# Performance work log

Hardware: AMD Instinct MI355X
Metric: run time of the kernel (lower is better)

## Reference

```python
import jax, jax.numpy as jnp
import numpy as np

N, E = 50000, 800000
IN, HID, HEADS, OUT = 128, 16, 4, 40
NEG_SLOPE = 0.2
BN_EPS = 1e-5


def gat_conv(x, edge_src, edge_dst, W, a_src, a_dst, b, heads, out_ch, concat):
    """PyG GATConv: linear -> per-head attention logits -> segment softmax over
    incoming edges of each target node -> weighted scatter-sum. Self-loops are
    assumed already appended to edge_src/edge_dst."""
    n = x.shape[0]
    h = (x @ W.T).reshape(n, heads, out_ch)              # [N, H, C]
    alpha_s = jnp.sum(h * a_src, axis=-1)                # [N, H]
    alpha_d = jnp.sum(h * a_dst, axis=-1)                # [N, H]
    logits = jax.nn.leaky_relu(alpha_s[edge_src] + alpha_d[edge_dst], NEG_SLOPE)  # [E', H]
    # numerically-stable segment softmax over edges grouped by target node
    seg_max = jax.ops.segment_max(logits, edge_dst, num_segments=n)
    e = jnp.exp(logits - seg_max[edge_dst])
    seg_sum = jax.ops.segment_sum(e, edge_dst, num_segments=n)
    alpha = e / (seg_sum[edge_dst] + 1e-16)              # [E', H]
    msg = h[edge_src] * alpha[:, :, None]                # [E', H, C]
    out = jax.ops.segment_sum(msg, edge_dst, num_segments=n)  # [N, H, C]
    out = out.reshape(n, heads * out_ch) if concat else out.mean(axis=1)
    return out + b


def batch_norm(x, gamma, beta):
    mean = x.mean(axis=0)
    var = x.var(axis=0)  # biased, matching torch BN normalization
    return (x - mean) * jax.lax.rsqrt(var + BN_EPS) * gamma + beta


def setup_inputs() -> dict:
    key = jax.random.key(0)
    ks = jax.random.split(key, 16)
    H = HID * HEADS  # 64
    inp = {
        "x": jax.random.normal(ks[0], (N, IN), jnp.float32),
        "edge_index": jax.random.randint(ks[1], (2, E), 0, N, jnp.int64),
        # layer 0: IN -> HID, HEADS heads, concat
        "W0": jax.random.normal(ks[2], (H, IN), jnp.float32) * 0.05,
        "a_src0": jax.random.normal(ks[3], (1, HEADS, HID), jnp.float32) * 0.05,
        "a_dst0": jax.random.normal(ks[4], (1, HEADS, HID), jnp.float32) * 0.05,
        "b0": jnp.zeros((H,), jnp.float32),
        # layer 1: H -> HID, HEADS heads, concat
        "W1": jax.random.normal(ks[5], (H, H), jnp.float32) * 0.05,
        "a_src1": jax.random.normal(ks[6], (1, HEADS, HID), jnp.float32) * 0.05,
        "a_dst1": jax.random.normal(ks[7], (1, HEADS, HID), jnp.float32) * 0.05,
        "b1": jnp.zeros((H,), jnp.float32),
        # layer 2: H -> OUT, 1 head, concat=False
        "W2": jax.random.normal(ks[8], (OUT, H), jnp.float32) * 0.05,
        "a_src2": jax.random.normal(ks[9], (1, 1, OUT), jnp.float32) * 0.05,
        "a_dst2": jax.random.normal(ks[10], (1, 1, OUT), jnp.float32) * 0.05,
        "b2": jnp.zeros((OUT,), jnp.float32),
        # batchnorms
        "g0": jnp.ones((H,), jnp.float32), "bt0": jnp.zeros((H,), jnp.float32),
        "g1": jnp.ones((H,), jnp.float32), "bt1": jnp.zeros((H,), jnp.float32),
    }
    return inp


def reference(x, edge_index, W0, a_src0, a_dst0, b0, W1, a_src1, a_dst1, b1,
              W2, a_src2, a_dst2, b2, g0, bt0, g1, bt1):
    n = x.shape[0]
    loop = jnp.arange(n, dtype=edge_index.dtype)
    src = jnp.concatenate([edge_index[0], loop])  # PyG add_self_loops=True
    dst = jnp.concatenate([edge_index[1], loop])

    h = gat_conv(x, src, dst, W0, a_src0, a_dst0, b0, HEADS, HID, True)
    h = batch_norm(h, g0, bt0)
    h = gat_conv(h, src, dst, W1, a_src1, a_dst1, b1, HEADS, HID, True)
    h = batch_norm(h, g1, bt1)
    emb = gat_conv(h, src, dst, W2, a_src2, a_dst2, b2, 1, OUT, False)
    return jax.nn.log_softmax(emb, axis=1), emb
```

## Files before the change

### kernel.cpp

```cpp
#include <hip/hip_runtime.h>
#include <hip/hip_bf16.h>
#include <math.h>

#define NN 50000
#define NE 800000
#define CURPAD 16
#define CAP 64

using short8 = __attribute__((ext_vector_type(8))) short;
using f32x4  = __attribute__((ext_vector_type(4))) float;

__device__ inline short bfbits(float f) {
    __hip_bfloat16 b = __float2bfloat16(f);
    return __builtin_bit_cast(short, b);
}
__device__ inline short8 cvt8(float4 lo, float4 hi) {
    short8 r;
    r[0] = bfbits(lo.x); r[1] = bfbits(lo.y); r[2] = bfbits(lo.z); r[3] = bfbits(lo.w);
    r[4] = bfbits(hi.x); r[5] = bfbits(hi.y); r[6] = bfbits(hi.z); r[7] = bfbits(hi.w);
    return r;
}

template<int K, int CT, int COUT, int HEADSN, bool FUSESCAT>
__global__ __launch_bounds__(256) void mfma_gemm(
    const float* __restrict__ x, const float* __restrict__ W,
    const float* __restrict__ a_src, const float* __restrict__ a_dst,
    const float* __restrict__ bnsc, const float* __restrict__ bnsh,
    ushort* __restrict__ h, float* __restrict__ as_out, float* __restrict__ ad_out,
    int n, int scat_blocks,
    const int* __restrict__ esrc, const int* __restrict__ edst,
    int* __restrict__ cnt, unsigned* __restrict__ pk2)
{
    if (FUSESCAT && (int)blockIdx.x < scat_blocks) {
        int base = ((int)blockIdx.x * 256 + (int)threadIdx.x) * 8;
        int d[8], pv[8];
#pragma unroll
        for (int j = 0; j < 8; j++)
            d[j] = (base + j < NE) ? edst[base + j] : -1;
#pragma unroll
        for (int j = 0; j < 8; j++)
            pv[j] = (d[j] >= 0) ? atomicAdd(&cnt[(size_t)d[j] * CURPAD], 1) : 0;
#pragma unroll
        for (int j = 0; j < 8; j++)
            if (d[j] >= 0 && pv[j] < CAP)
                pk2[((size_t)d[j] << 6) + pv[j]] = (unsigned)esrc[base + j];
        return;
    }

    int bid = (int)blockIdx.x - (FUSESCAT ? scat_blocks : 0);
    int tid = threadIdx.x;
    int w = tid >> 6, l = tid & 63;
    int l15 = l & 15, g = l >> 4;
    int m_base = bid * 64 + w * 16;

    f32x4 acc[CT];
#pragma unroll
    for (int ct = 0; ct < CT; ct++) acc[ct] = f32x4{0.f, 0.f, 0.f, 0.f};

    int arow = m_base + l15; if (arow >= n) arow = n - 1;
    const float* xrow = x + (size_t)arow * K;

#pragma unroll
    for (int ks = 0; ks < K / 32; ks++) {
        int k0 = ks * 32 + g * 8;
        float4 lo = *(const float4*)(xrow + k0);
        float4 hi = *(const float4*)(xrow + k0 + 4);
        if (bnsc) {
            float4 s0 = *(const float4*)(bnsc + k0), s1 = *(const float4*)(bnsc + k0 + 4);
            float4 t0 = *(const float4*)(bnsh + k0), t1 = *(const float4*)(bnsh + k0 + 4);
            lo.x = lo.x * s0.x + t0.x; lo.y = lo.y * s0.y + t0.y;
            lo.z = lo.z * s0.z + t0.z; lo.w = lo.w * s0.w + t0.w;
            hi.x = hi.x * s1.x + t1.x; hi.y = hi.y * s1.y + t1.y;
            hi.z = hi.z * s1.z + t1.z; hi.w = hi.w * s1.w + t1.w;
        }
        short8 a = cvt8(lo, hi);
#pragma unroll
        for (int ct = 0; ct < CT; ct++) {
            int wrow = ct * 16 + l15;
            if (wrow >= COUT) wrow = COUT - 1;
            const float* Wr = W + (size_t)wrow * K;
            float4 blo = *(const float4*)(Wr + k0);
            float4 bhi = *(const float4*)(Wr + k0 + 4);
            short8 b = cvt8(blo, bhi);
            acc[ct] = __builtin_amdgcn_mfma_f32_16x16x32_bf16(a, b, acc[ct], 0, 0, 0);
        }
    }

#pragma unroll
    for (int ct = 0; ct < CT; ct++) {
#pragma unroll
        for (int r = 0; r < 4; r++) {
            int row = m_base + g * 4 + r;
            int col = ct * 16 + l15;
            if (row < n && col < COUT)
                h[(size_t)row * COUT + col] = (ushort)bfbits(acc[ct][r]);
        }
    }

    if (HEADSN == 4) {
        float asv[CT], adv[CT];
#pragma unroll
        for (int ct = 0; ct < CT; ct++) {
            asv[ct] = a_src[ct * 16 + l15];
            adv[ct] = a_dst[ct * 16 + l15];
        }
#pragma unroll
        for (int r = 0; r < 4; r++) {
            float rs[CT], rd[CT];
#pragma unroll
            for (int ct = 0; ct < CT; ct++) {
                rs[ct] = acc[ct][r] * asv[ct];
                rd[ct] = acc[ct][r] * adv[ct];
            }
#pragma unroll
            for (int off = 1; off < 16; off <<= 1) {
#pragma unroll
                for (int ct = 0; ct < CT; ct++) {
                    rs[ct] += __shfl_xor(rs[ct], off);
                    rd[ct] += __shfl_xor(rd[ct], off);
                }
            }
            int row = m_base + g * 4 + r;
            if (row < n) {
#pragma unroll
                for (int ct = 0; ct < CT; ct++) {
                    if (l15 == ct) {
                        as_out[row * 4 + ct] = rs[ct];
                        ad_out[row * 4 + ct] = rd[ct];
                    }
                }
            }
        }
    } else {
        float asv[CT], adv[CT];
#pragma unroll
        for (int ct = 0; ct < CT; ct++) {
            int col = ct * 16 + l15;
            asv[ct] = (col < COUT) ? a_src[col] : 0.f;
            adv[ct] = (col < COUT) ? a_dst[col] : 0.f;
        }
#pragma unroll
        for (int r = 0; r < 4; r++) {
            float rs = 0.f, rd = 0.f;
#pragma unroll
            for (int ct = 0; ct < CT; ct++) {
                rs += acc[ct][r] * asv[ct];
                rd += acc[ct][r] * adv[ct];
            }
#pragma unroll
            for (int off = 1; off < 16; off <<= 1) {
                rs += __shfl_xor(rs, off);
                rd += __shfl_xor(rd, off);
            }
            int row = m_base + g * 4 + r;
            if (row < n && l15 == 0) {
                as_out[row] = rs;
                ad_out[row] = rd;
            }
        }
    }
}

template<int CH, int HEADSN, bool LSM>
__global__ __launch_bounds__(256) void gat_kernel(
    const ushort* __restrict__ h, const float* __restrict__ as,
    const float* __restrict__ ad, const int* __restrict__ cnt,
    const unsigned* __restrict__ pk2, const float* __restrict__ bias,
    float* __restrict__ out, int n)
{
    int wid = (blockIdx.x * blockDim.x + threadIdx.x) >> 6;
    int lane = threadIdx.x & 63;
    if (wid >= n) return;
    int sub = lane & 7, eslot = lane >> 3;
    int c0 = sub * 8;
    bool act = (c0 < CH);
    int hd = (HEADSN == 1) ? 0 : (sub >> 1);
    float adi = ad[wid * HEADSN + hd];

    double ac0 = 0, ac1 = 0, ac2 = 0, ac3 = 0, ac4 = 0, ac5 = 0, ac6 = 0, ac7 = 0;
    double ss = 0;

    int deg = cnt[(size_t)wid * CURPAD];
    if (deg > CAP) deg = CAP;
    int slotbase = wid << 6;
    int nit = (deg + 7) >> 3;
    int pos = eslot;
    bool ok = pos < deg;
    int s = 0; float av = 0.f;
    if (ok) { s = (int)pk2[slotbase + pos]; av = as[s * HEADSN + hd]; }
    for (int it = 0; it < nit; ++it) {
        int posn = pos + 8;
        bool ok2 = (it + 1 < nit) && (posn < deg);
        int s2 = 0; float av2 = 0.f;
        if (ok2) { s2 = (int)pk2[slotbase + posn]; av2 = as[s2 * HEADSN + hd]; }
        float p = 0.f;
        if (ok) {
            float lg = av + adi;
            lg = (lg > 0.f) ? lg : 0.2f * lg;
            p = __expf(fminf(lg, 60.f));
        }
        float h0 = 0.f, h1 = 0.f, h2 = 0.f, h3 = 0.f, h4 = 0.f, h5 = 0.f, h6 = 0.f, h7 = 0.f;
        if (act) {
            uint4 u = *(const uint4*)&h[(size_t)s * CH + c0];
            h0 = __uint_as_float((u.x & 0xffffu) << 16);
            h1 = __uint_as_float(u.x & 0xffff0000u);
            h2 = __uint_as_float((u.y & 0xffffu) << 16);
            h3 = __uint_as_float(u.y & 0xffff0000u);
            h4 = __uint_as_float((u.z & 0xffffu) << 16);
            h5 = __uint_as_float(u.z & 0xffff0000u);
            h6 = __uint_as_float((u.w & 0xffffu) << 16);
            h7 = __uint_as_float(u.w & 0xffff0000u);
        }
        ss += (double)p;
        ac0 += (double)p * (double)h0;  ac1 += (double)p * (double)h1;
        ac2 += (double)p * (double)h2;  ac3 += (double)p * (double)h3;
        ac4 += (double)p * (double)h4;  ac5 += (double)p * (double)h5;
        ac6 += (double)p * (double)h6;  ac7 += (double)p * (double)h7;
        s = s2; av = av2; ok = ok2; pos = posn;
    }

#pragma unroll
    for (int o = 8; o <= 32; o <<= 1) {
        ss  += __shfl_xor(ss, o);
        ac0 += __shfl_xor(ac0, o);  ac1 += __shfl_xor(ac1, o);
        ac2 += __shfl_xor(ac2, o);  ac3 += __shfl_xor(ac3, o);
        ac4 += __shfl_xor(ac4, o);  ac5 += __shfl_xor(ac5, o);
        ac6 += __shfl_xor(ac6, o);  ac7 += __shfl_xor(ac7, o);
    }

    {
        float lg = as[wid * HEADSN + hd] + adi;
        lg = (lg > 0.f) ? lg : 0.2f * lg;
        float ps = __expf(fminf(lg, 60.f));
        ss += (double)ps;
        if (act) {
            uint4 u = *(const uint4*)&h[(size_t)wid * CH + c0];
            ac0 += (double)ps * (double)__uint_as_float((u.x & 0xffffu) << 16);
            ac1 += (double)ps * (double)__uint_as_float(u.x & 0xffff0000u);
            ac2 += (double)ps * (double)__uint_as_float((u.y & 0xffffu) << 16);
            ac3 += (double)ps * (double)__uint_as_float(u.y & 0xffff0000u);
            ac4 += (double)ps * (double)__uint_as_float((u.z & 0xffffu) << 16);
            ac5 += (double)ps * (double)__uint_as_float(u.z & 0xffff0000u);
            ac6 += (double)ps * (double)__uint_as_float((u.w & 0xffffu) << 16);
            ac7 += (double)ps * (double)__uint_as_float(u.w & 0xffff0000u);
        }
    }

    double inv = 1.0 / (ss + 1e-16);
    float4 bv0 = make_float4(0.f, 0.f, 0.f, 0.f), bv1 = bv0;
    if (act) {
        bv0 = *(const float4*)&bias[c0];
        bv1 = *(const float4*)&bias[c0 + 4];
    }
    float v0 = (float)(ac0 * inv) + bv0.x;
    float v1 = (float)(ac1 * inv) + bv0.y;
    float v2 = (float)(ac2 * inv) + bv0.z;
    float v3 = (float)(ac3 * inv) + bv0.w;
    float v4 = (float)(ac4 * inv) + bv1.x;
    float v5 = (float)(ac5 * inv) + bv1.y;
    float v6 = (float)(ac6 * inv) + bv1.z;
    float v7 = (float)(ac7 * inv) + bv1.w;

    if (LSM) {
        float mx = act ? fmaxf(fmaxf(fmaxf(v0, v1), fmaxf(v2, v3)),
                               fmaxf(fmaxf(v4, v5), fmaxf(v6, v7))) : -INFINITY;
        for (int o = 4; o >= 1; o >>= 1) mx = fmaxf(mx, __shfl_xor(mx, o));
        float sse = 0.f;
        if (act)
            sse = __expf(v0 - mx) + __expf(v1 - mx) + __expf(v2 - mx) + __expf(v3 - mx)
                + __expf(v4 - mx) + __expf(v5 - mx) + __expf(v6 - mx) + __expf(v7 - mx);
        for (int o = 4; o >= 1; o >>= 1) sse += __shfl_xor(sse, o);
        float ls = logf(sse);
        if (eslot == 0 && act) {
            *(float4*)&out[(size_t)wid * CH + c0] =
                make_float4(v0 - mx - ls, v1 - mx - ls, v2 - mx - ls, v3 - mx - ls);
            *(float4*)&out[(size_t)wid * CH + c0 + 4] =
                make_float4(v4 - mx - ls, v5 - mx - ls, v6 - mx - ls, v7 - mx - ls);
            *(float4*)&out[(size_t)n * CH + (size_t)wid * CH + c0] =
                make_float4(v0, v1, v2, v3);
            *(float4*)&out[(size_t)n * CH + (size_t)wid * CH + c0 + 4] =
                make_float4(v4, v5, v6, v7);
        }
    } else {
        if (eslot == 0 && act) {
            *(float4*)&out[(size_t)wid * CH + c0] = make_float4(v0, v1, v2, v3);
            *(float4*)&out[(size_t)wid * CH + c0 + 4] = make_float4(v4, v5, v6, v7);
        }
    }
}

__global__ __launch_bounds__(256) void bn_stats(const float* __restrict__ B,
                                                float* __restrict__ psum,
                                                float* __restrict__ psq, int n) {
    __shared__ float ls[256], ls2[256];
    int tid = threadIdx.x;
    int c = tid & 63, r = tid >> 6;
    float s = 0.f, s2 = 0.f;
    for (int i = blockIdx.x * 4 + r; i < n; i += gridDim.x * 4) {
        float v = B[i * 64 + c];
        s += v; s2 += v * v;
    }
    ls[tid] = s; ls2[tid] = s2;
    __syncthreads();
    if (tid < 64) {
        s  = ls[tid] + ls[tid + 64] + ls[tid + 128] + ls[tid + 192];
        s2 = ls2[tid] + ls2[tid + 64] + ls2[tid + 128] + ls2[tid + 192];
        psum[blockIdx.x * 64 + tid] = s;
        psq[blockIdx.x * 64 + tid]  = s2;
    }
}

__global__ void bn_final(const float* __restrict__ psum, const float* __restrict__ psq,
                         const float* __restrict__ g, const float* __restrict__ bt,
                         float* __restrict__ sc, float* __restrict__ sh, int n) {
    int c = threadIdx.x;
    float s = 0.f, s2 = 0.f;
    for (int b = 0; b < 256; b++) {
        s  += psum[b * 64 + c];
        s2 += psq[b * 64 + c];
    }
    float mean = s / n;
    float var = s2 / n - mean * mean;
    float inv = rsqrtf(var + 1e-5f);
    float scale = g[c] * inv;
    sc[c] = scale;
    sh[c] = bt[c] - mean * scale;
}

extern "C" void kernel_launch(void* const* d_in, const int* in_sizes, int n_in,
                              void* d_out, int out_size, void* d_ws, size_t ws_size,
                              hipStream_t stream) {
    const float* x   = (const float*)d_in[0];
    const int*   ei  = (const int*)d_in[1];
    const float* W0  = (const float*)d_in[2];
    const float* as0 = (const float*)d_in[3];
    const float* ad0 = (const float*)d_in[4];
    const float* b0  = (const float*)d_in[5];
    const float* W1  = (const float*)d_in[6];
    const float* as1 = (const float*)d_in[7];
    const float* ad1 = (const float*)d_in[8];
    const float* b1  = (const float*)d_in[9];
    const float* W2  = (const float*)d_in[10];
    const float* as2 = (const float*)d_in[11];
    const float* ad2 = (const float*)d_in[12];
    const float* b2  = (const float*)d_in[13];
    const float* g0  = (const float*)d_in[14];
    const float* bt0 = (const float*)d_in[15];
    const float* g1  = (const float*)d_in[16];
    const float* bt1 = (const float*)d_in[17];

    const int* esrc = ei;
    const int* edst = ei + NE;

    char* ws = (char*)d_ws;
    size_t off = 0;
    auto alloc = [&](size_t bytes) {
        void* p = ws + off;
        off += (bytes + 255) & ~(size_t)255;
        return p;
    };
    int* cnt      = (int*)alloc((size_t)NN * CURPAD * 4);
    unsigned* pk2 = (unsigned*)alloc((size_t)NN * CAP * 4);
    ushort* hbuf  = (ushort*)alloc((size_t)NN * 64 * 2);
    float* obuf   = (float*)alloc((size_t)NN * 64 * 4);
    float* asb    = (float*)alloc((size_t)NN * 4 * 4);
    float* adb    = (float*)alloc((size_t)NN * 4 * 4);
    float* psum   = (float*)alloc(256 * 64 * 4);
    float* psq    = (float*)alloc(256 * 64 * 4);
    float* sc     = (float*)alloc(64 * 4);
    float* sh     = (float*)alloc(64 * 4);

    const int SCB = (NE + 2047) / 2048;
    const int GBM = (NN + 63) / 64;
    const int GB4 = (NN + 3) / 4;

    hipMemsetAsync(cnt, 0, (size_t)NN * CURPAD * 4, stream);
    mfma_gemm<128, 4, 64, 4, true><<<SCB + GBM, 256, 0, stream>>>(
        x, W0, as0, ad0, nullptr, nullptr, hbuf, asb, adb, NN, SCB,
        esrc, edst, cnt, pk2);

    gat_kernel<64, 4, false><<<GB4, 256, 0, stream>>>(hbuf, asb, adb, cnt, pk2,
                                                      b0, obuf, NN);

    bn_stats<<<256, 256, 0, stream>>>(obuf, psum, psq, NN);
    bn_final<<<1, 64, 0, stream>>>(psum, psq, g0, bt0, sc, sh, NN);

    mfma_gemm<64, 4, 64, 4, false><<<GBM, 256, 0, stream>>>(
        obuf, W1, as1, ad1, sc, sh, hbuf, asb, adb, NN, 0,
        nullptr, nullptr, nullptr, nullptr);
    gat_kernel<64, 4, false><<<GB4, 256, 0, stream>>>(hbuf, asb, adb, cnt, pk2,
                                                      b1, obuf, NN);

    bn_stats<<<256, 256, 0, stream>>>(obuf, psum, psq, NN);
    bn_final<<<1, 64, 0, stream>>>(psum, psq, g1, bt1, sc, sh, NN);

    mfma_gemm<64, 3, 40, 1, false><<<GBM, 256, 0, stream>>>(
        obuf, W2, as2, ad2, sc, sh, hbuf, asb, adb, NN, 0,
        nullptr, nullptr, nullptr, nullptr);
    gat_kernel<40, 1, true><<<GB4, 256, 0, stream>>>(hbuf, asb, adb, cnt, pk2,
                                                     b2, (float*)d_out, NN);
}
```

Before: 251.6 us.

## Fuse BN stats into GAT aggregation, widen per-lane channels to sixteen

Batch-norm partial sums are now computed inside the GAT aggregation kernel through shared memory. This removes the separate bn_stats pass over the 50000x64 output, and a new 64-block bn_reduce combines the per-block partials. The aggregation kernel now gives each lane 16 channels (4 lanes per node, 16 edge slots per iteration) instead of 8 channels across 8 slots, which doubles the edge parallelism per wave but also doubles the double-precision accumulator registers. The edge-source load in the scatter is hoisted next to the destination load. The trade-offs are higher register pressure, fewer channels active for the 40-channel layer (the last lane idles), and a grid that assumes N is divisible by 4.

New measurement: 386.6 us. 53.7% more time.

```diff
diff --git a/kernel.cpp b/kernel.cpp
--- a/kernel.cpp
+++ b/kernel.cpp
@@ -33,17 +33,19 @@
 {
     if (FUSESCAT && (int)blockIdx.x < scat_blocks) {
         int base = ((int)blockIdx.x * 256 + (int)threadIdx.x) * 8;
-        int d[8], pv[8];
-#pragma unroll
-        for (int j = 0; j < 8; j++)
+        int d[8], sv[8], pv[8];
+#pragma unroll
+        for (int j = 0; j < 8; j++) {
             d[j] = (base + j < NE) ? edst[base + j] : -1;
+            sv[j] = (base + j < NE) ? esrc[base + j] : 0;
+        }
 #pragma unroll
         for (int j = 0; j < 8; j++)
             pv[j] = (d[j] >= 0) ? atomicAdd(&cnt[(size_t)d[j] * CURPAD], 1) : 0;
 #pragma unroll
         for (int j = 0; j < 8; j++)
             if (d[j] >= 0 && pv[j] < CAP)
-                pk2[((size_t)d[j] << 6) + pv[j]] = (unsigned)esrc[base + j];
+                pk2[((size_t)d[j] << 6) + pv[j]] = (unsigned)sv[j];
         return;
     }
 
@@ -161,35 +163,44 @@
     }
 }
 
-template<int CH, int HEADSN, bool LSM>
+__device__ inline float bfh(unsigned u, bool hi) {
+    return __uint_as_float(hi ? (u & 0xffff0000u) : ((u & 0xffffu) << 16));
+}
+
+template<int CH, int HEADSN, bool LSM, bool BNP>
 __global__ __launch_bounds__(256) void gat_kernel(
     const ushort* __restrict__ h, const float* __restrict__ as,
     const float* __restrict__ ad, const int* __restrict__ cnt,
     const unsigned* __restrict__ pk2, const float* __restrict__ bias,
-    float* __restrict__ out, int n)
+    float* __restrict__ out, float* __restrict__ psum, float* __restrict__ psq,
+    int n)
 {
-    int wid = (blockIdx.x * blockDim.x + threadIdx.x) >> 6;
-    int lane = threadIdx.x & 63;
-    if (wid >= n) return;
-    int sub = lane & 7, eslot = lane >> 3;
-    int c0 = sub * 8;
-    bool act = (c0 < CH);
-    int hd = (HEADSN == 1) ? 0 : (sub >> 1);
+    __shared__ float lsv[4][64];
+    int tid = threadIdx.x;
+    int w = tid >> 6;
+    int wid = blockIdx.x * 4 + w;
+    int lane = tid & 63;
+    int sub = lane & 3, eslot = lane >> 2;
+    int c0 = sub * 16;
+    bool act0 = (c0 < CH), act1 = (c0 + 8 < CH);
+    int hd = (HEADSN == 1) ? 0 : sub;
     float adi = ad[wid * HEADSN + hd];
 
-    double ac0 = 0, ac1 = 0, ac2 = 0, ac3 = 0, ac4 = 0, ac5 = 0, ac6 = 0, ac7 = 0;
-    double ss = 0;
+    double acc[16];
+#pragma unroll
+    for (int j = 0; j < 16; j++) acc[j] = 0.0;
+    double ss = 0.0;
 
     int deg = cnt[(size_t)wid * CURPAD];
     if (deg > CAP) deg = CAP;
     int slotbase = wid << 6;
-    int nit = (deg + 7) >> 3;
+    int nit = (deg + 15) >> 4;
     int pos = eslot;
     bool ok = pos < deg;
     int s = 0; float av = 0.f;
     if (ok) { s = (int)pk2[slotbase + pos]; av = as[s * HEADSN + hd]; }
     for (int it = 0; it < nit; ++it) {
-        int posn = pos + 8;
+        int posn = pos + 16;
         bool ok2 = (it + 1 < nit) && (posn < deg);
         int s2 = 0; float av2 = 0.f;
         if (ok2) { s2 = (int)pk2[slotbase + posn]; av2 = as[s2 * HEADSN + hd]; }
@@ -199,33 +210,26 @@
             lg = (lg > 0.f) ? lg : 0.2f * lg;
             p = __expf(fminf(lg, 60.f));
         }
-        float h0 = 0.f, h1 = 0.f, h2 = 0.f, h3 = 0.f, h4 = 0.f, h5 = 0.f, h6 = 0.f, h7 = 0.f;
-        if (act) {
-            uint4 u = *(const uint4*)&h[(size_t)s * CH + c0];
-            h0 = __uint_as_float((u.x & 0xffffu) << 16);
-            h1 = __uint_as_float(u.x & 0xffff0000u);
-            h2 = __uint_as_float((u.y & 0xffffu) << 16);
-            h3 = __uint_as_float(u.y & 0xffff0000u);
-            h4 = __uint_as_float((u.z & 0xffffu) << 16);
-            h5 = __uint_as_float(u.z & 0xffff0000u);
-            h6 = __uint_as_float((u.w & 0xffffu) << 16);
-            h7 = __uint_as_float(u.w & 0xffff0000u);
-        }
+        uint4 ua = make_uint4(0, 0, 0, 0), ub = ua;
+        if (act0) ua = *(const uint4*)&h[(size_t)s * CH + c0];
+        if (act1) ub = *(const uint4*)&h[(size_t)s * CH + c0 + 8];
         ss += (double)p;
-        ac0 += (double)p * (double)h0;  ac1 += (double)p * (double)h1;
-        ac2 += (double)p * (double)h2;  ac3 += (double)p * (double)h3;
-        ac4 += (double)p * (double)h4;  ac5 += (double)p * (double)h5;
-        ac6 += (double)p * (double)h6;  ac7 += (double)p * (double)h7;
+        acc[0] += (double)p * (double)bfh(ua.x, 0); acc[1] += (double)p * (double)bfh(ua.x, 1);
+        acc[2] += (double)p * (double)bfh(ua.y, 0); acc[3] += (double)p * (double)bfh(ua.y, 1);
+        acc[4] += (double)p * (double)bfh(ua.z, 0); acc[5] += (double)p * (double)bfh(ua.z, 1);
+        acc[6] += (double)p * (double)bfh(ua.w, 0); acc[7] += (double)p * (double)bfh(ua.w, 1);
+        acc[8] += (double)p * (double)bfh(ub.x, 0); acc[9] += (double)p * (double)bfh(ub.x, 1);
+        acc[10] += (double)p * (double)bfh(ub.y, 0); acc[11] += (double)p * (double)bfh(ub.y, 1);
+        acc[12] += (double)p * (double)bfh(ub.z, 0); acc[13] += (double)p * (double)bfh(ub.z, 1);
+        acc[14] += (double)p * (double)bfh(ub.w, 0); acc[15] += (double)p * (double)bfh(ub.w, 1);
         s = s2; av = av2; ok = ok2; pos = posn;
     }
 
 #pragma unroll
-    for (int o = 8; o <= 32; o <<= 1) {
-        ss  += __shfl_xor(ss, o);
-        ac0 += __shfl_xor(ac0, o);  ac1 += __shfl_xor(ac1, o);
-        ac2 += __shfl_xor(ac2, o);  ac3 += __shfl_xor(ac3, o);
-        ac4 += __shfl_xor(ac4, o);  ac5 += __shfl_xor(ac5, o);
-        ac6 += __shfl_xor(ac6, o);  ac7 += __shfl_xor(ac7, o);
+    for (int o = 4; o <= 32; o <<= 1) {
+        ss += __shfl_xor(ss, o);
+#pragma unroll
+        for (int j = 0; j < 16; j++) acc[j] += __shfl_xor(acc[j], o);
     }
 
     {
@@ -233,98 +237,110 @@
         lg = (lg > 0.f) ? lg : 0.2f * lg;
         float ps = __expf(fminf(lg, 60.f));
         ss += (double)ps;
-        if (act) {
-            uint4 u = *(const uint4*)&h[(size_t)wid * CH + c0];
-            ac0 += (double)ps * (double)__uint_as_float((u.x & 0xffffu) << 16);
-            ac1 += (double)ps * (double)__uint_as_float(u.x & 0xffff0000u);
-            ac2 += (double)ps * (double)__uint_as_float((u.y & 0xffffu) << 16);
-            ac3 += (double)ps * (double)__uint_as_float(u.y & 0xffff0000u);
-            ac4 += (double)ps * (double)__uint_as_float((u.z & 0xffffu) << 16);
-            ac5 += (double)ps * (double)__uint_as_float(u.z & 0xffff0000u);
-            ac6 += (double)ps * (double)__uint_as_float((u.w & 0xffffu) << 16);
-            ac7 += (double)ps * (double)__uint_as_float(u.w & 0xffff0000u);
-        }
+        uint4 ua = make_uint4(0, 0, 0, 0), ub = ua;
+        if (act0) ua = *(const uint4*)&h[(size_t)wid * CH + c0];
+        if (act1) ub = *(const uint4*)&h[(size_t)wid * CH + c0 + 8];
+        acc[0] += (double)ps * (double)bfh(ua.x, 0); acc[1] += (double)ps * (double)bfh(ua.x, 1);
+        acc[2] += (double)ps * (double)bfh(ua.y, 0); acc[3] += (double)ps * (double)bfh(ua.y, 1);
+        acc[4] += (double)ps * (double)bfh(ua.z, 0); acc[5] += (double)ps * (double)bfh(ua.z, 1);
+        acc[6] += (double)ps * (double)bfh(ua.w, 0); acc[7] += (double)ps * (double)bfh(ua.w, 1);
+        acc[8] += (double)ps * (double)bfh(ub.x, 0); acc[9] += (double)ps * (double)bfh(ub.x, 1);
+        acc[10] += (double)ps * (double)bfh(ub.y, 0); acc[11] += (double)ps * (double)bfh(ub.y, 1);
+        acc[12] += (double)ps * (double)bfh(ub.z, 0); acc[13] += (double)ps * (double)bfh(ub.z, 1);
+        acc[14] += (double)ps * (double)bfh(ub.w, 0); acc[15] += (double)ps * (double)bfh(ub.w, 1);
     }
 
     double inv = 1.0 / (ss + 1e-16);
-    float4 bv0 = make_float4(0.f, 0.f, 0.f, 0.f), bv1 = bv0;
-    if (act) {
-        bv0 = *(const float4*)&bias[c0];
-        bv1 = *(const float4*)&bias[c0 + 4];
-    }
-    float v0 = (float)(ac0 * inv) + bv0.x;
-    float v1 = (float)(ac1 * inv) + bv0.y;
-    float v2 = (float)(ac2 * inv) + bv0.z;
-    float v3 = (float)(ac3 * inv) + bv0.w;
-    float v4 = (float)(ac4 * inv) + bv1.x;
-    float v5 = (float)(ac5 * inv) + bv1.y;
-    float v6 = (float)(ac6 * inv) + bv1.z;
-    float v7 = (float)(ac7 * inv) + bv1.w;
+    float v[16];
+    float4 bv[4];
+#pragma unroll
+    for (int k = 0; k < 4; k++) {
+        bool a = (k < 2) ? act0 : act1;
+        bv[k] = a ? *(const float4*)&bias[c0 + k * 4] : make_float4(0.f, 0.f, 0.f, 0.f);
+    }
+#pragma unroll
+    for (int j = 0; j < 16; j++)
+        v[j] = (float)(acc[j] * inv) + ((const float*)bv)[j];
+
+    if (BNP) {
+        if (eslot == 0) {
+#pragma unroll
+            for (int j = 0; j < 16; j++) lsv[w][c0 + j] = v[j];
+        }
+        __syncthreads();
+        if (tid < 64) {
+            float sV = lsv[0][tid] + lsv[1][tid] + lsv[2][tid] + lsv[3][tid];
+            float sQ = lsv[0][tid] * lsv[0][tid] + lsv[1][tid] * lsv[1][tid]
+                     + lsv[2][tid] * lsv[2][tid] + lsv[3][tid] * lsv[3][tid];
+            psum[(size_t)blockIdx.x * 64 + tid] = sV;
+            psq[(size_t)blockIdx.x * 64 + tid]  = sQ;
+        }
+    }
 
     if (LSM) {
-        float mx = act ? fmaxf(fmaxf(fmaxf(v0, v1), fmaxf(v2, v3)),
-                               fmaxf(fmaxf(v4, v5), fmaxf(v6, v7))) : -INFINITY;
-        for (int o = 4; o >= 1; o >>= 1) mx = fmaxf(mx, __shfl_xor(mx, o));
+        float mx = -INFINITY;
+#pragma unroll
+        for (int j = 0; j < 16; j++)
+            if ((j < 8) ? act0 : act1) mx = fmaxf(mx, v[j]);
+        for (int o = 2; o >= 1; o >>= 1) mx = fmaxf(mx, __shfl_xor(mx, o));
         float sse = 0.f;
-        if (act)
-            sse = __expf(v0 - mx) + __expf(v1 - mx) + __expf(v2 - mx) + __expf(v3 - mx)
-                + __expf(v4 - mx) + __expf(v5 - mx) + __expf(v6 - mx) + __expf(v7 - mx);
-        for (int o = 4; o >= 1; o >>= 1) sse += __shfl_xor(sse, o);
+#pragma unroll
+        for (int j = 0; j < 16; j++)
+            if ((j < 8) ? act0 : act1) sse += __expf(v[j] - mx);
+        for (int o = 2; o >= 1; o >>= 1) sse += __shfl_xor(sse, o);
         float ls = logf(sse);
-        if (eslot == 0 && act) {
-            *(float4*)&out[(size_t)wid * CH + c0] =
-                make_float4(v0 - mx - ls, v1 - mx - ls, v2 - mx - ls, v3 - mx - ls);
-            *(float4*)&out[(size_t)wid * CH + c0 + 4] =
-                make_float4(v4 - mx - ls, v5 - mx - ls, v6 - mx - ls, v7 - mx - ls);
-            *(float4*)&out[(size_t)n * CH + (size_t)wid * CH + c0] =
-                make_float4(v0, v1, v2, v3);
-            *(float4*)&out[(size_t)n * CH + (size_t)wid * CH + c0 + 4] =
-                make_float4(v4, v5, v6, v7);
+        if (eslot == 0) {
+#pragma unroll
+            for (int k = 0; k < 4; k++) {
+                bool a = (k < 2) ? act0 : act1;
+                if (a) {
+                    float4 r = make_float4(v[k*4] - mx - ls, v[k*4+1] - mx - ls,
+                                           v[k*4+2] - mx - ls, v[k*4+3] - mx - ls);
+                    *(float4*)&out[(size_t)wid * CH + c0 + k * 4] = r;
+                    float4 emb = make_float4(v[k*4], v[k*4+1], v[k*4+2], v[k*4+3]);
+                    *(float4*)&out[(size_t)n * CH + (size_t)wid * CH + c0 + k * 4] = emb;
+                }
+            }
         }
     } else {
-        if (eslot == 0 && act) {
-            *(float4*)&out[(size_t)wid * CH + c0] = make_float4(v0, v1, v2, v3);
-            *(float4*)&out[(size_t)wid * CH + c0 + 4] = make_float4(v4, v5, v6, v7);
-        }
-    }
-}
-
-__global__ __launch_bounds__(256) void bn_stats(const float* __restrict__ B,
-                                                float* __restrict__ psum,
-                                                float* __restrict__ psq, int n) {
-    __shared__ float ls[256], ls2[256];
-    int tid = threadIdx.x;
-    int c = tid & 63, r = tid >> 6;
+        if (eslot == 0) {
+#pragma unroll
+            for (int k = 0; k < 4; k++) {
+                bool a = (k < 2) ? act0 : act1;
+                if (a)
+                    *(float4*)&out[(size_t)wid * CH + c0 + k * 4] =
+                        make_float4(v[k*4], v[k*4+1], v[k*4+2], v[k*4+3]);
+            }
+        }
+    }
+}
+
+__global__ __launch_bounds__(256) void bn_reduce(
+    const float* __restrict__ psum, const float* __restrict__ psq,
+    const float* __restrict__ g, const float* __restrict__ bt,
+    float* __restrict__ sc, float* __restrict__ sh, int nb, int n)
+{
+    int c = blockIdx.x;
+    int t = threadIdx.x;
     float s = 0.f, s2 = 0.f;
-    for (int i = blockIdx.x * 4 + r; i < n; i += gridDim.x * 4) {
-        float v = B[i * 64 + c];
-        s += v; s2 += v * v;
-    }
-    ls[tid] = s; ls2[tid] = s2;
-    __syncthreads();
-    if (tid < 64) {
-        s  = ls[tid] + ls[tid + 64] + ls[tid + 128] + ls[tid + 192];
-        s2 = ls2[tid] + ls2[tid + 64] + ls2[tid + 128] + ls2[tid + 192];
-        psum[blockIdx.x * 64 + tid] = s;
-        psq[blockIdx.x * 64 + tid]  = s2;
-    }
-}
-
-__global__ void bn_final(const float* __restrict__ psum, const float* __restrict__ psq,
-                         const float* __restrict__ g, const float* __restrict__ bt,
-                         float* __restrict__ sc, float* __restrict__ sh, int n) {
-    int c = threadIdx.x;
-    float s = 0.f, s2 = 0.f;
-    for (int b = 0; b < 256; b++) {
-        s  += psum[b * 64 + c];
-        s2 += psq[b * 64 + c];
-    }
-    float mean = s / n;
-    float var = s2 / n - mean * mean;
-    float inv = rsqrtf(var + 1e-5f);
-    float scale = g[c] * inv;
-    sc[c] = scale;
-    sh[c] = bt[c] - mean * scale;
+    for (int r = t; r < nb; r += 256) {
+        s  += psum[(size_t)r * 64 + c];
+        s2 += psq[(size_t)r * 64 + c];
+    }
+    __shared__ float a[256], b[256];
+    a[t] = s; b[t] = s2; __syncthreads();
+    for (int o = 128; o >= 1; o >>= 1) {
+        if (t < o) { a[t] += a[t + o]; b[t] += b[t + o]; }
+        __syncthreads();
+    }
+    if (t == 0) {
+        float mean = a[0] / n;
+        float var = b[0] / n - mean * mean;
+        float invs = rsqrtf(var + 1e-5f);
+        float scale = g[c] * invs;
+        sc[c] = scale;
+        sh[c] = bt[c] - mean * scale;
+    }
 }
 
 extern "C" void kernel_launch(void* const* d_in, const int* in_sizes, int n_in,
@@ -365,38 +381,34 @@
     float* obuf   = (float*)alloc((size_t)NN * 64 * 4);
     float* asb    = (float*)alloc((size_t)NN * 4 * 4);
     float* adb    = (float*)alloc((size_t)NN * 4 * 4);
-    float* psum   = (float*)alloc(256 * 64 * 4);
-    float* psq    = (float*)alloc(256 * 64 * 4);
+    float* psum   = (float*)alloc((size_t)(NN / 4) * 64 * 4);
+    float* psq    = (float*)alloc((size_t)(NN / 4) * 64 * 4);
     float* sc     = (float*)alloc(64 * 4);
     float* sh     = (float*)alloc(64 * 4);
 
     const int SCB = (NE + 2047) / 2048;
     const int GBM = (NN + 63) / 64;
-    const int GB4 = (NN + 3) / 4;
+    const int GB4 = NN / 4;
 
     hipMemsetAsync(cnt, 0, (size_t)NN * CURPAD * 4, stream);
     mfma_gemm<128, 4, 64, 4, true><<<SCB + GBM, 256, 0, stream>>>(
         x, W0, as0, ad0, nullptr, nullptr, hbuf, asb, adb, NN, SCB,
         esrc, edst, cnt, pk2);
 
-    gat_kernel<64, 4, false><<<GB4, 256, 0, stream>>>(hbuf, asb, adb, cnt, pk2,
-                                                      b0, obuf, NN);
-
-    bn_stats<<<256, 256, 0, stream>>>(obuf, psum, psq, NN);
-    bn_final<<<1, 64, 0, stream>>>(psum, psq, g0, bt0, sc, sh, NN);
+    gat_kernel<64, 4, false, true><<<GB4, 256, 0, stream>>>(
+        hbuf, asb, adb, cnt, pk2, b0, obuf, psum, psq, NN);
+    bn_reduce<<<64, 256, 0, stream>>>(psum, psq, g0, bt0, sc, sh, GB4, NN);
 
     mfma_gemm<64, 4, 64, 4, false><<<GBM, 256, 0, stream>>>(
         obuf, W1, as1, ad1, sc, sh, hbuf, asb, adb, NN, 0,
         nullptr, nullptr, nullptr, nullptr);
-    gat_kernel<64, 4, false><<<GB4, 256, 0, stream>>>(hbuf, asb, adb, cnt, pk2,
-                                                      b1, obuf, NN);
-
-    bn_stats<<<256, 256, 0, stream>>>(obuf, psum, psq, NN);
-    bn_final<<<1, 64, 0, stream>>>(psum, psq, g1, bt1, sc, sh, NN);
+    gat_kernel<64, 4, false, true><<<GB4, 256, 0, stream>>>(
+        hbuf, asb, adb, cnt, pk2, b1, obuf, psum, psq, NN);
+    bn_reduce<<<64, 256, 0, stream>>>(psum, psq, g1, bt1, sc, sh, GB4, NN);
 
     mfma_gemm<64, 3, 40, 1, false><<<GBM, 256, 0, stream>>>(
         obuf, W2, as2, ad2, sc, sh, hbuf, asb, adb, NN, 0,
         nullptr, nullptr, nullptr, nullptr);
-    gat_kernel<40, 1, true><<<GB4, 256, 0, stream>>>(hbuf, asb, adb, cnt, pk2,
-                                                     b2, (float*)d_out, NN);
-}
+    gat_kernel<40, 1, true, false><<<GB4, 256, 0, stream>>>(
+        hbuf, asb, adb, cnt, pk2, b2, (float*)d_out, nullptr, nullptr, NN);
+}
```

## Fuse BN partial stats into GAT kernel and switch accumulation to fp32

Applied to the files above, without the earlier changes.

Batch-norm partial sums and sums of squares are now computed inside the GAT aggregation kernel through a per-block shared-memory reduction. A parallel bn_reduce kernel replaces the separate bn_stats and bn_final kernels, which removes a full re-read of the 50000x64 output and one launch per layer. The GAT accumulators move from double to float, avoiding slow FP64 arithmetic and shuffles at some cost in precision. The scatter path also preloads esrc alongside edst, and the grid now assumes N is divisible by 4.

Result: no change. 252.8 us (+0.5%).

```diff
diff --git a/kernel.cpp b/kernel.cpp
--- a/kernel.cpp
+++ b/kernel.cpp
@@ -33,17 +33,19 @@
 {
     if (FUSESCAT && (int)blockIdx.x < scat_blocks) {
         int base = ((int)blockIdx.x * 256 + (int)threadIdx.x) * 8;
-        int d[8], pv[8];
-#pragma unroll
-        for (int j = 0; j < 8; j++)
+        int d[8], sv[8], pv[8];
+#pragma unroll
+        for (int j = 0; j < 8; j++) {
             d[j] = (base + j < NE) ? edst[base + j] : -1;
+            sv[j] = (base + j < NE) ? esrc[base + j] : 0;
+        }
 #pragma unroll
         for (int j = 0; j < 8; j++)
             pv[j] = (d[j] >= 0) ? atomicAdd(&cnt[(size_t)d[j] * CURPAD], 1) : 0;
 #pragma unroll
         for (int j = 0; j < 8; j++)
             if (d[j] >= 0 && pv[j] < CAP)
-                pk2[((size_t)d[j] << 6) + pv[j]] = (unsigned)esrc[base + j];
+                pk2[((size_t)d[j] << 6) + pv[j]] = (unsigned)sv[j];
         return;
     }
 
@@ -161,24 +163,28 @@
     }
 }
 
-template<int CH, int HEADSN, bool LSM>
+template<int CH, int HEADSN, bool LSM, bool BNP>
 __global__ __launch_bounds__(256) void gat_kernel(
     const ushort* __restrict__ h, const float* __restrict__ as,
     const float* __restrict__ ad, const int* __restrict__ cnt,
     const unsigned* __restrict__ pk2, const float* __restrict__ bias,
-    float* __restrict__ out, int n)
+    float* __restrict__ out, float* __restrict__ psum, float* __restrict__ psq,
+    int n)
 {
-    int wid = (blockIdx.x * blockDim.x + threadIdx.x) >> 6;
-    int lane = threadIdx.x & 63;
-    if (wid >= n) return;
+    __shared__ float lsv[4][64];
+    int tid = threadIdx.x;
+    int w = tid >> 6;
+    int wid = blockIdx.x * 4 + w;
+    int lane = tid & 63;
     int sub = lane & 7, eslot = lane >> 3;
     int c0 = sub * 8;
     bool act = (c0 < CH);
     int hd = (HEADSN == 1) ? 0 : (sub >> 1);
     float adi = ad[wid * HEADSN + hd];
 
-    double ac0 = 0, ac1 = 0, ac2 = 0, ac3 = 0, ac4 = 0, ac5 = 0, ac6 = 0, ac7 = 0;
-    double ss = 0;
+    float ac0 = 0.f, ac1 = 0.f, ac2 = 0.f, ac3 = 0.f;
+    float ac4 = 0.f, ac5 = 0.f, ac6 = 0.f, ac7 = 0.f;
+    float ss = 0.f;
 
     int deg = cnt[(size_t)wid * CURPAD];
     if (deg > CAP) deg = CAP;
@@ -211,11 +217,9 @@
             h6 = __uint_as_float((u.w & 0xffffu) << 16);
             h7 = __uint_as_float(u.w & 0xffff0000u);
         }
-        ss += (double)p;
-        ac0 += (double)p * (double)h0;  ac1 += (double)p * (double)h1;
-        ac2 += (double)p * (double)h2;  ac3 += (double)p * (double)h3;
-        ac4 += (double)p * (double)h4;  ac5 += (double)p * (double)h5;
-        ac6 += (double)p * (double)h6;  ac7 += (double)p * (double)h7;
+        ss += p;
+        ac0 += p * h0;  ac1 += p * h1;  ac2 += p * h2;  ac3 += p * h3;
+        ac4 += p * h4;  ac5 += p * h5;  ac6 += p * h6;  ac7 += p * h7;
         s = s2; av = av2; ok = ok2; pos = posn;
     }
 
@@ -232,34 +236,49 @@
         float lg = as[wid * HEADSN + hd] + adi;
         lg = (lg > 0.f) ? lg : 0.2f * lg;
         float ps = __expf(fminf(lg, 60.f));
-        ss += (double)ps;
+        ss += ps;
         if (act) {
             uint4 u = *(const uint4*)&h[(size_t)wid * CH + c0];
-            ac0 += (double)ps * (double)__uint_as_float((u.x & 0xffffu) << 16);
-            ac1 += (double)ps * (double)__uint_as_float(u.x & 0xffff0000u);
-            ac2 += (double)ps * (double)__uint_as_float((u.y & 0xffffu) << 16);
-            ac3 += (double)ps * (double)__uint_as_float(u.y & 0xffff0000u);
-            ac4 += (double)ps * (double)__uint_as_float((u.z & 0xffffu) << 16);
-            ac5 += (double)ps * (double)__uint_as_float(u.z & 0xffff0000u);
-            ac6 += (double)ps * (double)__uint_as_float((u.w & 0xffffu) << 16);
-            ac7 += (double)ps * (double)__uint_as_float(u.w & 0xffff0000u);
-        }
-    }
-
-    double inv = 1.0 / (ss + 1e-16);
+            ac0 += ps * __uint_as_float((u.x & 0xffffu) << 16);
+            ac1 += ps * __uint_as_float(u.x & 0xffff0000u);
+            ac2 += ps * __uint_as_float((u.y & 0xffffu) << 16);
+            ac3 += ps * __uint_as_float(u.y & 0xffff0000u);
+            ac4 += ps * __uint_as_float((u.z & 0xffffu) << 16);
+            ac5 += ps * __uint_as_float(u.z & 0xffff0000u);
+            ac6 += ps * __uint_as_float((u.w & 0xffffu) << 16);
+            ac7 += ps * __uint_as_float(u.w & 0xffff0000u);
+        }
+    }
+
+    float inv = 1.f / (ss + 1e-16f);
     float4 bv0 = make_float4(0.f, 0.f, 0.f, 0.f), bv1 = bv0;
     if (act) {
         bv0 = *(const float4*)&bias[c0];
         bv1 = *(const float4*)&bias[c0 + 4];
     }
-    float v0 = (float)(ac0 * inv) + bv0.x;
-    float v1 = (float)(ac1 * inv) + bv0.y;
-    float v2 = (float)(ac2 * inv) + bv0.z;
-    float v3 = (float)(ac3 * inv) + bv0.w;
-    float v4 = (float)(ac4 * inv) + bv1.x;
-    float v5 = (float)(ac5 * inv) + bv1.y;
-    float v6 = (float)(ac6 * inv) + bv1.z;
-    float v7 = (float)(ac7 * inv) + bv1.w;
+    float v0 = ac0 * inv + bv0.x;
+    float v1 = ac1 * inv + bv0.y;
+    float v2 = ac2 * inv + bv0.z;
+    float v3 = ac3 * inv + bv0.w;
+    float v4 = ac4 * inv + bv1.x;
+    float v5 = ac5 * inv + bv1.y;
+    float v6 = ac6 * inv + bv1.z;
+    float v7 = ac7 * inv + bv1.w;
+
+    if (BNP) {
+        if (eslot == 0) {
+            lsv[w][c0 + 0] = v0; lsv[w][c0 + 1] = v1;
+            lsv[w][c0 + 2] = v2; lsv[w][c0 + 3] = v3;
+            lsv[w][c0 + 4] = v4; lsv[w][c0 + 5] = v5;
+            lsv[w][c0 + 6] = v6; lsv[w][c0 + 7] = v7;
+        }
+        __syncthreads();
+        if (tid < 64) {
+            float a0 = lsv[0][tid], a1 = lsv[1][tid], a2 = lsv[2][tid], a3 = lsv[3][tid];
+            psum[(size_t)blockIdx.x * 64 + tid] = (a0 + a1) + (a2 + a3);
+            psq[(size_t)blockIdx.x * 64 + tid]  = (a0 * a0 + a1 * a1) + (a2 * a2 + a3 * a3);
+        }
+    }
 
     if (LSM) {
         float mx = act ? fmaxf(fmaxf(fmaxf(v0, v1), fmaxf(v2, v3)),
@@ -289,42 +308,32 @@
     }
 }
 
-__global__ __launch_bounds__(256) void bn_stats(const float* __restrict__ B,
-                                                float* __restrict__ psum,
-                                                float* __restrict__ psq, int n) {
-    __shared__ float ls[256], ls2[256];
-    int tid = threadIdx.x;
-    int c = tid & 63, r = tid >> 6;
+__global__ __launch_bounds__(256) void bn_reduce(
+    const float* __restrict__ psum, const float* __restrict__ psq,
+    const float* __restrict__ g, const float* __restrict__ bt,
+    float* __restrict__ sc, float* __restrict__ sh, int nb, int n)
+{
+    int c = blockIdx.x;
+    int t = threadIdx.x;
     float s = 0.f, s2 = 0.f;
-    for (int i = blockIdx.x * 4 + r; i < n; i += gridDim.x * 4) {
-        float v = B[i * 64 + c];
-        s += v; s2 += v * v;
-    }
-    ls[tid] = s; ls2[tid] = s2;
-    __syncthreads();
-    if (tid < 64) {
-        s  = ls[tid] + ls[tid + 64] + ls[tid + 128] + ls[tid + 192];
-        s2 = ls2[tid] + ls2[tid + 64] + ls2[tid + 128] + ls2[tid + 192];
-        psum[blockIdx.x * 64 + tid] = s;
-        psq[blockIdx.x * 64 + tid]  = s2;
-    }
-}
-
-__global__ void bn_final(const float* __restrict__ psum, const float* __restrict__ psq,
-                         const float* __restrict__ g, const float* __restrict__ bt,
-                         float* __restrict__ sc, float* __restrict__ sh, int n) {
-    int c = threadIdx.x;
-    float s = 0.f, s2 = 0.f;
-    for (int b = 0; b < 256; b++) {
-        s  += psum[b * 64 + c];
-        s2 += psq[b * 64 + c];
-    }
-    float mean = s / n;
-    float var = s2 / n - mean * mean;
-    float inv = rsqrtf(var + 1e-5f);
-    float scale = g[c] * inv;
-    sc[c] = scale;
-    sh[c] = bt[c] - mean * scale;
+    for (int r = t; r < nb; r += 256) {
+        s  += psum[(size_t)r * 64 + c];
+        s2 += psq[(size_t)r * 64 + c];
+    }
+    __shared__ float a[256], b[256];
+    a[t] = s; b[t] = s2; __syncthreads();
+    for (int o = 128; o >= 1; o >>= 1) {
+        if (t < o) { a[t] += a[t + o]; b[t] += b[t + o]; }
+        __syncthreads();
+    }
+    if (t == 0) {
+        float mean = a[0] / n;
+        float var = b[0] / n - mean * mean;
+        float invs = rsqrtf(var + 1e-5f);
+        float scale = g[c] * invs;
+        sc[c] = scale;
+        sh[c] = bt[c] - mean * scale;
+    }
 }
 
 extern "C" void kernel_launch(void* const* d_in, const int* in_sizes, int n_in,
@@ -365,38 +374,34 @@
     float* obuf   = (float*)alloc((size_t)NN * 64 * 4);
     float* asb    = (float*)alloc((size_t)NN * 4 * 4);
     float* adb    = (float*)alloc((size_t)NN * 4 * 4);
-    float* psum   = (float*)alloc(256 * 64 * 4);
-    float* psq    = (float*)alloc(256 * 64 * 4);
+    float* psum   = (float*)alloc((size_t)(NN / 4) * 64 * 4);
+    float* psq    = (float*)alloc((size_t)(NN / 4) * 64 * 4);
     float* sc     = (float*)alloc(64 * 4);
     float* sh     = (float*)alloc(64 * 4);
 
     const int SCB = (NE + 2047) / 2048;
     const int GBM = (NN + 63) / 64;
-    const int GB4 = (NN + 3) / 4;
+    const int GB4 = NN / 4;
 
     hipMemsetAsync(cnt, 0, (size_t)NN * CURPAD * 4, stream);
     mfma_gemm<128, 4, 64, 4, true><<<SCB + GBM, 256, 0, stream>>>(
         x, W0, as0, ad0, nullptr, nullptr, hbuf, asb, adb, NN, SCB,
         esrc, edst, cnt, pk2);
 
-    gat_kernel<64, 4, false><<<GB4, 256, 0, stream>>>(hbuf, asb, adb, cnt, pk2,
-                                                      b0, obuf, NN);
-
-    bn_stats<<<256, 256, 0, stream>>>(obuf, psum, psq, NN);
-    bn_final<<<1, 64, 0, stream>>>(psum, psq, g0, bt0, sc, sh, NN);
+    gat_kernel<64, 4, false, true><<<GB4, 256, 0, stream>>>(
+        hbuf, asb, adb, cnt, pk2, b0, obuf, psum, psq, NN);
+    bn_reduce<<<64, 256, 0, stream>>>(psum, psq, g0, bt0, sc, sh, GB4, NN);
 
     mfma_gemm<64, 4, 64, 4, false><<<GBM, 256, 0, stream>>>(
         obuf, W1, as1, ad1, sc, sh, hbuf, asb, adb, NN, 0,
         nullptr, nullptr, nullptr, nullptr);
-    gat_kernel<64, 4, false><<<GB4, 256, 0, stream>>>(hbuf, asb, adb, cnt, pk2,
-                                                      b1, obuf, NN);
-
-    bn_stats<<<256, 256, 0, stream>>>(obuf, psum, psq, NN);
-    bn_final<<<1, 64, 0, stream>>>(psum, psq, g1, bt1, sc, sh, NN);
+    gat_kernel<64, 4, false, true><<<GB4, 256, 0, stream>>>(
+        hbuf, asb, adb, cnt, pk2, b1, obuf, psum, psq, NN);
+    bn_reduce<<<64, 256, 0, stream>>>(psum, psq, g1, bt1, sc, sh, GB4, NN);
 
     mfma_gemm<64, 3, 40, 1, false><<<GBM, 256, 0, stream>>>(
         obuf, W2, as2, ad2, sc, sh, hbuf, asb, adb, NN, 0,
         nullptr, nullptr, nullptr, nullptr);
-    gat_kernel<40, 1, true><<<GB4, 256, 0, stream>>>(hbuf, asb, adb, cnt, pk2,
-                                                     b2, (float*)d_out, NN);
-}
+    gat_kernel<40, 1, true, false><<<GB4, 256, 0, stream>>>(
+        hbuf, asb, adb, cnt, pk2, b2, (float*)d_out, nullptr, nullptr, NN);
+}
```
